# Kernel optimization log

Hardware: AMD Instinct MI355X
Metric: run time of the kernel (lower is better)

The kernel has to match this reference:

```python
import jax, jax.numpy as jnp
import numpy as np

W_SIZE = 16
WIN = 2 * W_SIZE + 1
OUT_F = 256
MODEL = 512  # output_features * 2


def setup_inputs() -> dict:
    key = jax.random.key(0)
    ks = jax.random.split(key, 7)
    B, T = 4, 2048
    s = 0.02
    return {
        "x": jax.random.normal(ks[0], (B, T, MODEL), jnp.float32),
        "encoder_outputs": jax.random.normal(ks[1], (B, T, OUT_F), jnp.float32),
        # Attention: attn Linear (OUT_F + MODEL -> OUT_F), v Linear (OUT_F -> 1, no bias)
        "W_attn": jax.random.normal(ks[2], (OUT_F + MODEL, OUT_F), jnp.float32) * s,
        "b_attn": jnp.zeros((OUT_F,), jnp.float32),
        "v": jax.random.normal(ks[3], (OUT_F,), jnp.float32) * s,
        # final linear: (MODEL + OUT_F -> OUT_F)
        "W_lin": jax.random.normal(ks[4], (MODEL + OUT_F, OUT_F), jnp.float32) * s,
        "b_lin": jnp.zeros((OUT_F,), jnp.float32),
    }


def _windows(enc):
    B, T, F = enc.shape
    padded = jnp.pad(enc, ((0, 0), (W_SIZE, W_SIZE), (0, 0)))
    idx = jnp.arange(T)[:, None] + jnp.arange(WIN)[None, :]
    return padded[:, idx]


def reference(x, encoder_outputs, W_attn, b_attn, v, W_lin, b_lin):
    win = _windows(encoder_outputs)
    B, T, W, F = win.shape
    # additive (Bahdanau) score: concat(hidden, window) -> Linear -> tanh -> v
    Wh, We = W_attn[:MODEL], W_attn[MODEL:]
    energy = jnp.tanh(
        jnp.einsum('btm,mo->bto', x, Wh)[:, :, None, :]
        + jnp.einsum('btwf,fo->btwo', win, We)
        + b_attn
    )
    scores = jnp.einsum('btwo,o->btw', energy, v)
    a = jax.nn.softmax(scores, axis=-1)
    weighted = jnp.einsum('btw,btwf->btf', a, win)        # [B, T, F]
    h = jnp.concatenate([x, weighted], axis=-1)           # [B, T, MODEL+F]
    out = jax.nn.sigmoid(jnp.einsum('btk,ko->bto', h, W_lin) + b_lin)
    return out, a[:, :, None, :]
```

## Files before the change

kernel.cpp:

```cpp
#include <hip/hip_runtime.h>
#include <math.h>

#define T_DIM 2048
#define B_DIM 4
#define BT (B_DIM * T_DIM)
#define MODEL 512
#define OUTF 256
#define WSZ 16
#define WIN 33

#define BM 128
#define BN 128
#define BK 32

#define TB 16
#define HALO 48
#define TS 72

#define ESCALE 2.885390081777927f
#define ECLAMP 30.0f

typedef __attribute__((ext_vector_type(8))) short bf16x8;
typedef __attribute__((ext_vector_type(4))) float f32x4;

__device__ inline unsigned short f2bf(float f) {
  unsigned int u = __float_as_uint(f);
  u += 0x7fffu + ((u >> 16) & 1u);
  return (unsigned short)(u >> 16);
}
__device__ inline float bflo(unsigned int u) {
  return __uint_as_float(u << 16);
}
__device__ inline float bfhi(unsigned int u) {
  return __uint_as_float(u & 0xffff0000u);
}
__device__ inline float bfs(unsigned short u) {
  return __uint_as_float(((unsigned int)u) << 16);
}
__device__ inline float fast_sigmoid(float z) {
  return __builtin_amdgcn_rcpf(1.f + __expf(-z));
}

template <int KS, int MODE>
__device__ __forceinline__ void gemm_body(
    unsigned short (*As)[BM * 40], unsigned short (*Bs)[BN * 40], int rb,
    const float* __restrict__ A, int lda,
    const float* __restrict__ W_attn, const float* __restrict__ W_lin,
    const float* __restrict__ b_attn, const float* __restrict__ b_lin,
    unsigned short* __restrict__ outb, unsigned short* __restrict__ outb2) {
  const int tid = threadIdx.x;
  const int cbg = rb >> 6, rp = rb & 63;
  const int row0 = rp * BM;
  const float* Wsrc = (cbg < 2) ? W_attn : W_lin;
  const int colw = (cbg & 1) * 128;
  constexpr int wrow0 = (MODE == 0) ? 0 : 512;

  const int arow = tid >> 2, akp = (tid & 3) * 8;
  const int brow = tid >> 4, bcp = (tid & 15) * 8;
  const int bkey = (bcp >> 3) & 3;
  const float* aptr = A + (size_t)(row0 + arow) * lda + akp;
  const float* bptr = Wsrc + (size_t)(wrow0 + brow) * OUTF + colw + bcp;

  float4 ra0[2], ra1[2], rb0[2], rb1[2];
  auto LOADS = [&](int sl, int ks) {
    const float* ap = aptr + ks * BK;
    ra0[sl] = *(const float4*)ap;
    ra1[sl] = *(const float4*)(ap + 4);
    const float* bp = bptr + (size_t)ks * BK * OUTF;
    rb0[sl] = *(const float4*)bp;
    rb1[sl] = *(const float4*)(bp + 4);
  };
  auto WRITE = [&](int sl, int buf) {
    unsigned short t[8] = {f2bf(ra0[sl].x), f2bf(ra0[sl].y), f2bf(ra0[sl].z),
                           f2bf(ra0[sl].w), f2bf(ra1[sl].x), f2bf(ra1[sl].y),
                           f2bf(ra1[sl].z), f2bf(ra1[sl].w)};
    *(uint4*)&As[buf][arow * 40 + akp] = *(const uint4*)t;
    const int bk = brow ^ (bkey << 3);
    Bs[buf][(bcp + 0) * 40 + bk] = f2bf(rb0[sl].x);
    Bs[buf][(bcp + 1) * 40 + bk] = f2bf(rb0[sl].y);
    Bs[buf][(bcp + 2) * 40 + bk] = f2bf(rb0[sl].z);
    Bs[buf][(bcp + 3) * 40 + bk] = f2bf(rb0[sl].w);
    Bs[buf][(bcp + 4) * 40 + bk] = f2bf(rb1[sl].x);
    Bs[buf][(bcp + 5) * 40 + bk] = f2bf(rb1[sl].y);
    Bs[buf][(bcp + 6) * 40 + bk] = f2bf(rb1[sl].z);
    Bs[buf][(bcp + 7) * 40 + bk] = f2bf(rb1[sl].w);
  };

  const int w = tid >> 6, lane = tid & 63;
  const int lr = lane & 15, kg = lane >> 4;
  const int rbase = (w & 3) * 32;
  const int cbase = (w >> 2) * 64;
  int bo[4];
#pragma unroll
  for (int f = 0; f < 4; ++f) {
    const int bc = cbase + f * 16 + lr;
    bo[f] = bc * 40 + ((kg ^ ((bc >> 3) & 3)) << 3);
  }

  f32x4 acc[2][4];
#pragma unroll
  for (int m = 0; m < 2; ++m)
#pragma unroll
    for (int f = 0; f < 4; ++f) acc[m][f] = {0.f, 0.f, 0.f, 0.f};

  LOADS(0, 0);
  if (KS > 1) LOADS(1, 1);
  WRITE(0, 0);
  __syncthreads();

#pragma unroll
  for (int ks = 0; ks < KS; ++ks) {
    if (ks + 2 < KS) LOADS(ks & 1, ks + 2);
    const int bf = ks & 1;
    bf16x8 a0 = *(const bf16x8*)&As[bf][(rbase + lr) * 40 + kg * 8];
    bf16x8 a1 = *(const bf16x8*)&As[bf][(rbase + 16 + lr) * 40 + kg * 8];
#pragma unroll
    for (int f = 0; f < 4; ++f) {
      bf16x8 bb = *(const bf16x8*)&Bs[bf][bo[f]];
      acc[0][f] = __builtin_amdgcn_mfma_f32_16x16x32_bf16(a0, bb, acc[0][f], 0, 0, 0);
      acc[1][f] = __builtin_amdgcn_mfma_f32_16x16x32_bf16(a1, bb, acc[1][f], 0, 0, 0);
    }
    if (ks + 1 < KS) WRITE((ks + 1) & 1, (ks + 1) & 1);
    __syncthreads();
  }

#pragma unroll
  for (int m = 0; m < 2; ++m) {
#pragma unroll
    for (int f = 0; f < 4; ++f) {
      const int col = (cbg & 1) * 128 + cbase + f * 16 + lr;
#pragma unroll
      for (int r = 0; r < 4; ++r) {
        const int row = row0 + rbase + m * 16 + kg * 4 + r;
        const float val = acc[m][f][r];
        if (MODE == 0) {
          if (cbg < 2) {
            const float y = fminf((val + b_attn[col]) * ESCALE, ECLAMP);
            outb[(size_t)row * OUTF + col] = f2bf(__builtin_amdgcn_exp2f(y));
          } else {
            outb2[(size_t)row * OUTF + col] = f2bf(val + b_lin[col]);
          }
        } else {
          if (cbg < 2) {
            const float y = fminf(val * ESCALE, ECLAMP);
            outb[(size_t)row * OUTF + col] = f2bf(__builtin_amdgcn_exp2f(y));
          } else {
            outb2[(size_t)row * OUTF + col] = f2bf(val);
          }
        }
      }
    }
  }
}

__global__ __launch_bounds__(512) void gemmAB_kernel(
    const float* __restrict__ x, const float* __restrict__ enc,
    const float* __restrict__ W_attn, const float* __restrict__ W_lin,
    const float* __restrict__ b_attn, const float* __restrict__ b_lin,
    unsigned short* __restrict__ xwe2, unsigned short* __restrict__ z1b,
    unsigned short* __restrict__ ewe2, unsigned short* __restrict__ encWl2) {
  __shared__ unsigned short As[2][BM * 40];
  __shared__ unsigned short Bs[2][BN * 40];
  if (blockIdx.x < 256)
    gemm_body<16, 0>(As, Bs, blockIdx.x, x, MODEL, W_attn, W_lin, b_attn,
                     b_lin, xwe2, z1b);
  else
    gemm_body<8, 1>(As, Bs, blockIdx.x - 256, enc, OUTF, W_attn, W_lin,
                    nullptr, nullptr, ewe2, encWl2);
}

__global__ __launch_bounds__(512) void attn_gemmc_kernel(
    const unsigned short* __restrict__ xwe2,
    const unsigned short* __restrict__ ewe2,
    const unsigned short* __restrict__ encWl2, const float* __restrict__ v,
    const unsigned short* __restrict__ z1b, float* __restrict__ out,
    float* __restrict__ a_out) {
  __shared__ unsigned short EwT[256 * TS];
  __shared__ unsigned short Ab[TB * TS];

  const int tid = threadIdx.x;
  const int wv = tid >> 6, lane = tid & 63;
  const int rb = ((blockIdx.x & 7) << 6) | (blockIdx.x >> 3);
  const int t0 = rb * TB;
  const int b = t0 >> 11;
  const int tloc = t0 & (T_DIM - 1);
  const int g = lane >> 4, sl = lane & 15;

  if (tid < TB * TS / 8) ((uint4*)Ab)[tid] = make_uint4(0, 0, 0, 0);
  {
    const int col = tid >> 1, off = 48 + (tid & 1) * 8;
    const int kswz = ((col >> 3) & 7) << 3;
    *(uint4*)&EwT[col * TS + (off ^ kswz)] = make_uint4(0, 0, 0, 0);
  }

  for (int u = tid; u < HALO * 32; u += 512) {
    const int r = u >> 5, s = u & 31;
    const int tg = tloc - WSZ + r;
    uint4 qw = make_uint4(0, 0, 0, 0);
    if ((unsigned)tg < T_DIM)
      qw = *(const uint4*)(encWl2 + (((size_t)(b * T_DIM + tg)) << 8) + s * 8);
    unsigned short tt[8];
    *(uint4*)tt = qw;
    const int rsw = r ^ ((s & 7) << 3);
#pragma unroll
    for (int j = 0; j < 8; ++j) EwT[(s * 8 + j) * TS + rsw] = tt[j];
  }

  float vf[16];
  {
    const float4* vp = (const float4*)(v + sl * 16);
#pragma unroll
    for (int j = 0; j < 4; ++j) {
      float4 t4 = vp[j];
      vf[4 * j] = t4.x; vf[4 * j + 1] = t4.y;
      vf[4 * j + 2] = t4.z; vf[4 * j + 3] = t4.w;
    }
  }
  __syncthreads();

  const int lrow = wv * 2;
  const int bt0 = t0 + lrow, bt1 = bt0 + 1;

  float xe0[16], xe1[16];
  {
    const uint4* xp0 = (const uint4*)(xwe2 + ((size_t)bt0 << 8) + sl * 16);
    const uint4* xp1 = (const uint4*)(xwe2 + ((size_t)bt1 << 8) + sl * 16);
    uint4 q0 = xp0[0], q1 = xp0[1], q2 = xp1[0], q3 = xp1[1];
    unsigned int u0[8] = {q0.x, q0.y, q0.z, q0.w, q1.x, q1.y, q1.z, q1.w};
    unsigned int u1[8] = {q2.x, q2.y, q2.z, q2.w, q3.x, q3.y, q3.z, q3.w};
#pragma unroll
    for (int j = 0; j < 8; ++j) {
      xe0[2 * j] = bflo(u0[j]); xe0[2 * j + 1] = bfhi(u0[j]);
      xe1[2 * j] = bflo(u1[j]); xe1[2 * j + 1] = bfhi(u1[j]);
    }
  }

  const size_t bbase = ((size_t)(b * T_DIM)) << 8;
  const int tb0 = tloc + lrow - WSZ;
  float s0 = 0.f, s1 = 0.f;
#pragma unroll
  for (int c = 0; c < 9; ++c) {
    const int w_ = c * 4 + g;
    const int tg0 = tb0 + w_, tg1 = tg0 + 1;
    const bool vr0 = ((unsigned)tg0 < T_DIM);
    const bool vr1 = ((unsigned)tg1 < T_DIM);
    const uint4* p0 =
        (const uint4*)(ewe2 + bbase + (((size_t)(vr0 ? tg0 : 0)) << 8) + sl * 16);
    const uint4* p1 =
        (const uint4*)(ewe2 + bbase + (((size_t)(vr1 ? tg1 : 0)) << 8) + sl * 16);
    uint4 a0q = p0[0], a1q = p0[1];
    uint4 b0q = p1[0], b1q = p1[1];
    const uint4 ones =
        make_uint4(0x3f803f80u, 0x3f803f80u, 0x3f803f80u, 0x3f803f80u);
    if (!vr0) { a0q = ones; a1q = ones; }
    if (!vr1) { b0q = ones; b1q = ones; }
    unsigned int e0[8] = {a0q.x, a0q.y, a0q.z, a0q.w, a1q.x, a1q.y, a1q.z, a1q.w};
    unsigned int e1[8] = {b0q.x, b0q.y, b0q.z, b0q.w, b1q.x, b1q.y, b1q.z, b1q.w};
    float acc0 = 0.f, acc1 = 0.f;
#pragma unroll
    for (int j = 0; j < 8; ++j) {
      const float v0 = vf[2 * j], v1 = vf[2 * j + 1];
      const float vsj = v0 + v1;
      {
        const float E0 = xe0[2 * j] * bflo(e0[j]);
        const float E1 = xe0[2 * j + 1] * bfhi(e0[j]);
        const float den = (E0 + 1.f) * (E1 + 1.f);
        float num = fmaf(v0, E1, vsj);
        num = fmaf(v1, E0, num);
        acc0 = fmaf(num, __builtin_amdgcn_rcpf(den), acc0);
      }
      {
        const float E0 = xe1[2 * j] * bflo(e1[j]);
        const float E1 = xe1[2 * j + 1] * bfhi(e1[j]);
        const float den = (E0 + 1.f) * (E1 + 1.f);
        float num = fmaf(v0, E1, vsj);
        num = fmaf(v1, E0, num);
        acc1 = fmaf(num, __builtin_amdgcn_rcpf(den), acc1);
      }
    }
#pragma unroll
    for (int off = 1; off < 16; off <<= 1) {
      acc0 += __shfl_xor(acc0, off);
      acc1 += __shfl_xor(acc1, off);
    }
    const int src = (lane & 3) << 4;
    float c0v = __shfl(acc0, src), c1v = __shfl(acc1, src);
    if ((lane >> 2) == c) { s0 = c0v; s1 = c1v; }
  }

  float p0 = (lane < WIN) ? __builtin_amdgcn_exp2f(-ESCALE * s0) : 0.f;
  float p1 = (lane < WIN) ? __builtin_amdgcn_exp2f(-ESCALE * s1) : 0.f;
  float q0 = p0, q1 = p1;
#pragma unroll
  for (int off = 1; off < 64; off <<= 1) {
    q0 += __shfl_xor(q0, off);
    q1 += __shfl_xor(q1, off);
  }
  const float a0v = p0 * __builtin_amdgcn_rcpf(q0);
  const float a1v = p1 * __builtin_amdgcn_rcpf(q1);
  if (lane < WIN) {
    a_out[(size_t)bt0 * WIN + lane] = a0v;
    a_out[(size_t)bt1 * WIN + lane] = a1v;
    Ab[lrow * TS + lrow + lane] = f2bf(a0v);
    Ab[(lrow + 1) * TS + (lrow + 1) + lane] = f2bf(a1v);
  }
  __syncthreads();

  const int lr = lane & 15, kg = lane >> 4;
  f32x4 acc[2] = {{0.f, 0.f, 0.f, 0.f}, {0.f, 0.f, 0.f, 0.f}};
#pragma unroll
  for (int ks = 0; ks < 2; ++ks) {
    bf16x8 a = *(const bf16x8*)&Ab[lr * TS + ks * 32 + kg * 8];
#pragma unroll
    for (int f = 0; f < 2; ++f) {
      const int colB = wv * 32 + f * 16 + lr;
      const int kswz = ((colB >> 3) & 7) << 3;
      bf16x8 bb = *(const bf16x8*)&EwT[colB * TS + ((ks * 32 + kg * 8) ^ kswz)];
      acc[f] = __builtin_amdgcn_mfma_f32_16x16x32_bf16(a, bb, acc[f], 0, 0, 0);
    }
  }
#pragma unroll
  for (int f = 0; f < 2; ++f) {
    const int col = wv * 32 + f * 16 + lr;
#pragma unroll
    for (int r = 0; r < 4; ++r) {
      const int row = t0 + kg * 4 + r;
      out[(size_t)row * OUTF + col] = fast_sigmoid(
          acc[f][r] + bfs(z1b[(size_t)row * OUTF + col]));
    }
  }
}

extern "C" void kernel_launch(void* const* d_in, const int* in_sizes, int n_in,
                              void* d_out, int out_size, void* d_ws,
                              size_t ws_size, hipStream_t stream) {
  const float* x      = (const float*)d_in[0];
  const float* enc    = (const float*)d_in[1];
  const float* W_attn = (const float*)d_in[2];
  const float* b_attn = (const float*)d_in[3];
  const float* v      = (const float*)d_in[4];
  const float* W_lin  = (const float*)d_in[5];
  const float* b_lin  = (const float*)d_in[6];

  float* out   = (float*)d_out;
  float* a_out = out + (size_t)BT * OUTF;

  unsigned short* xwe2   = (unsigned short*)d_ws;
  unsigned short* ewe2   = xwe2 + (size_t)BT * OUTF;
  unsigned short* encWl2 = ewe2 + (size_t)BT * OUTF;
  unsigned short* z1b    = encWl2 + (size_t)BT * OUTF;

  gemmAB_kernel<<<512, 512, 0, stream>>>(x, enc, W_attn, W_lin, b_attn,
                                         b_lin, xwe2, z1b, ewe2, encWl2);
  attn_gemmc_kernel<<<512, 512, 0, stream>>>(xwe2, ewe2, encWl2, v, z1b,
                                             out, a_out);
}
```

Measured before the change: 43.73 us.

## Remap attention score computation to one lane per window position

Reworks the score stage so each lane owns one window position (32 positions for two rows per wave) and loops over all 256 features serially, instead of 16-lane groups splitting the feature dimension and reducing with shuffles over 9 chunks. The x-projection row and v/paired-v vectors are staged in shared memory, and the 33rd window position is handled by a separate 16-lane reduction. This removes most cross-lane shuffle reductions and the wasted lanes of the 9x4 chunking, but each lane now makes strided global row reads and the kernel uses more LDS.

```diff
diff --git a/kernel.cpp b/kernel.cpp
--- a/kernel.cpp
+++ b/kernel.cpp
@@ -177,6 +177,9 @@
     float* __restrict__ a_out) {
   __shared__ unsigned short EwT[256 * TS];
   __shared__ unsigned short Ab[TB * TS];
+  __shared__ unsigned short Xe[TB * 256];
+  __shared__ float Vs[256];
+  __shared__ float Vp[128];
 
   const int tid = threadIdx.x;
   const int wv = tid >> 6, lane = tid & 63;
@@ -184,7 +187,6 @@
   const int t0 = rb * TB;
   const int b = t0 >> 11;
   const int tloc = t0 & (T_DIM - 1);
-  const int g = lane >> 4, sl = lane & 15;
 
   if (tid < TB * TS / 8) ((uint4*)Ab)[tid] = make_uint4(0, 0, 0, 0);
   {
@@ -205,104 +207,144 @@
 #pragma unroll
     for (int j = 0; j < 8; ++j) EwT[(s * 8 + j) * TS + rsw] = tt[j];
   }
-
-  float vf[16];
   {
-    const float4* vp = (const float4*)(v + sl * 16);
-#pragma unroll
-    for (int j = 0; j < 4; ++j) {
-      float4 t4 = vp[j];
-      vf[4 * j] = t4.x; vf[4 * j + 1] = t4.y;
-      vf[4 * j + 2] = t4.z; vf[4 * j + 3] = t4.w;
-    }
-  }
+    const int row = tid >> 5, seg = tid & 31;
+    *(uint4*)&Xe[row * 256 + seg * 8] =
+        *(const uint4*)(xwe2 + (((size_t)(t0 + row)) << 8) + seg * 8);
+  }
+  if (tid < 256) Vs[tid] = v[tid];
+  if (tid < 128) Vp[tid] = v[2 * tid] + v[2 * tid + 1];
   __syncthreads();
 
-  const int lrow = wv * 2;
-  const int bt0 = t0 + lrow, bt1 = bt0 + 1;
-
-  float xe0[16], xe1[16];
+  const size_t bbase = ((size_t)(b * T_DIM)) << 8;
+  const uint4 ones =
+      make_uint4(0x3f803f80u, 0x3f803f80u, 0x3f803f80u, 0x3f803f80u);
+
+  const int p = lane >> 5;
+  const int wA = (lane & 31) + 1;
+  const int lrow = wv * 2 + p;
+  const int bt = t0 + lrow;
+
+  float S = 0.f;
   {
-    const uint4* xp0 = (const uint4*)(xwe2 + ((size_t)bt0 << 8) + sl * 16);
-    const uint4* xp1 = (const uint4*)(xwe2 + ((size_t)bt1 << 8) + sl * 16);
-    uint4 q0 = xp0[0], q1 = xp0[1], q2 = xp1[0], q3 = xp1[1];
-    unsigned int u0[8] = {q0.x, q0.y, q0.z, q0.w, q1.x, q1.y, q1.z, q1.w};
-    unsigned int u1[8] = {q2.x, q2.y, q2.z, q2.w, q3.x, q3.y, q3.z, q3.w};
-#pragma unroll
-    for (int j = 0; j < 8; ++j) {
-      xe0[2 * j] = bflo(u0[j]); xe0[2 * j + 1] = bfhi(u0[j]);
-      xe1[2 * j] = bflo(u1[j]); xe1[2 * j + 1] = bfhi(u1[j]);
-    }
-  }
-
-  const size_t bbase = ((size_t)(b * T_DIM)) << 8;
-  const int tb0 = tloc + lrow - WSZ;
-  float s0 = 0.f, s1 = 0.f;
-#pragma unroll
-  for (int c = 0; c < 9; ++c) {
-    const int w_ = c * 4 + g;
-    const int tg0 = tb0 + w_, tg1 = tg0 + 1;
-    const bool vr0 = ((unsigned)tg0 < T_DIM);
-    const bool vr1 = ((unsigned)tg1 < T_DIM);
-    const uint4* p0 =
-        (const uint4*)(ewe2 + bbase + (((size_t)(vr0 ? tg0 : 0)) << 8) + sl * 16);
-    const uint4* p1 =
-        (const uint4*)(ewe2 + bbase + (((size_t)(vr1 ? tg1 : 0)) << 8) + sl * 16);
-    uint4 a0q = p0[0], a1q = p0[1];
-    uint4 b0q = p1[0], b1q = p1[1];
-    const uint4 ones =
-        make_uint4(0x3f803f80u, 0x3f803f80u, 0x3f803f80u, 0x3f803f80u);
-    if (!vr0) { a0q = ones; a1q = ones; }
-    if (!vr1) { b0q = ones; b1q = ones; }
-    unsigned int e0[8] = {a0q.x, a0q.y, a0q.z, a0q.w, a1q.x, a1q.y, a1q.z, a1q.w};
-    unsigned int e1[8] = {b0q.x, b0q.y, b0q.z, b0q.w, b1q.x, b1q.y, b1q.z, b1q.w};
-    float acc0 = 0.f, acc1 = 0.f;
-#pragma unroll
-    for (int j = 0; j < 8; ++j) {
-      const float v0 = vf[2 * j], v1 = vf[2 * j + 1];
-      const float vsj = v0 + v1;
-      {
-        const float E0 = xe0[2 * j] * bflo(e0[j]);
-        const float E1 = xe0[2 * j + 1] * bfhi(e0[j]);
-        const float den = (E0 + 1.f) * (E1 + 1.f);
-        float num = fmaf(v0, E1, vsj);
-        num = fmaf(v1, E0, num);
-        acc0 = fmaf(num, __builtin_amdgcn_rcpf(den), acc0);
-      }
-      {
-        const float E0 = xe1[2 * j] * bflo(e1[j]);
-        const float E1 = xe1[2 * j + 1] * bfhi(e1[j]);
-        const float den = (E0 + 1.f) * (E1 + 1.f);
-        float num = fmaf(v0, E1, vsj);
-        num = fmaf(v1, E0, num);
-        acc1 = fmaf(num, __builtin_amdgcn_rcpf(den), acc1);
-      }
-    }
-#pragma unroll
-    for (int off = 1; off < 16; off <<= 1) {
-      acc0 += __shfl_xor(acc0, off);
-      acc1 += __shfl_xor(acc1, off);
-    }
-    const int src = (lane & 3) << 4;
-    float c0v = __shfl(acc0, src), c1v = __shfl(acc1, src);
-    if ((lane >> 2) == c) { s0 = c0v; s1 = c1v; }
-  }
-
-  float p0 = (lane < WIN) ? __builtin_amdgcn_exp2f(-ESCALE * s0) : 0.f;
-  float p1 = (lane < WIN) ? __builtin_amdgcn_exp2f(-ESCALE * s1) : 0.f;
-  float q0 = p0, q1 = p1;
-#pragma unroll
-  for (int off = 1; off < 64; off <<= 1) {
-    q0 += __shfl_xor(q0, off);
-    q1 += __shfl_xor(q1, off);
-  }
-  const float a0v = p0 * __builtin_amdgcn_rcpf(q0);
-  const float a1v = p1 * __builtin_amdgcn_rcpf(q1);
-  if (lane < WIN) {
-    a_out[(size_t)bt0 * WIN + lane] = a0v;
-    a_out[(size_t)bt1 * WIN + lane] = a1v;
-    Ab[lrow * TS + lrow + lane] = f2bf(a0v);
-    Ab[(lrow + 1) * TS + (lrow + 1) + lane] = f2bf(a1v);
+    const int trow = tloc + lrow + wA - WSZ;
+    const bool vld = ((unsigned)trow < T_DIM);
+    const unsigned short* ewp =
+        ewe2 + bbase + (((size_t)(vld ? trow : 0)) << 8);
+#pragma unroll 4
+    for (int g = 0; g < 32; ++g) {
+      uint4 q = *(const uint4*)(ewp + g * 8);
+      if (!vld) q = ones;
+      const uint4 xq = *(const uint4*)&Xe[lrow * 256 + g * 8];
+      const float4 va = *(const float4*)&Vs[g * 8];
+      const float4 vb = *(const float4*)&Vs[g * 8 + 4];
+      const float4 vp4 = *(const float4*)&Vp[g * 4];
+      {
+        const float E0 = bflo(xq.x) * bflo(q.x);
+        const float E1 = bfhi(xq.x) * bfhi(q.x);
+        const float den = (E0 + 1.f) * (E1 + 1.f);
+        float num = fmaf(va.x, E1, vp4.x);
+        num = fmaf(va.y, E0, num);
+        S = fmaf(num, __builtin_amdgcn_rcpf(den), S);
+      }
+      {
+        const float E0 = bflo(xq.y) * bflo(q.y);
+        const float E1 = bfhi(xq.y) * bfhi(q.y);
+        const float den = (E0 + 1.f) * (E1 + 1.f);
+        float num = fmaf(va.z, E1, vp4.y);
+        num = fmaf(va.w, E0, num);
+        S = fmaf(num, __builtin_amdgcn_rcpf(den), S);
+      }
+      {
+        const float E0 = bflo(xq.z) * bflo(q.z);
+        const float E1 = bfhi(xq.z) * bfhi(q.z);
+        const float den = (E0 + 1.f) * (E1 + 1.f);
+        float num = fmaf(vb.x, E1, vp4.z);
+        num = fmaf(vb.y, E0, num);
+        S = fmaf(num, __builtin_amdgcn_rcpf(den), S);
+      }
+      {
+        const float E0 = bflo(xq.w) * bflo(q.w);
+        const float E1 = bfhi(xq.w) * bfhi(q.w);
+        const float den = (E0 + 1.f) * (E1 + 1.f);
+        float num = fmaf(vb.z, E1, vp4.w);
+        num = fmaf(vb.w, E0, num);
+        S = fmaf(num, __builtin_amdgcn_rcpf(den), S);
+      }
+    }
+  }
+
+  float accm = 0.f;
+  {
+    const int grp = lane >> 4, slm = lane & 15;
+    const int lrm = wv * 2 + (grp & 1);
+    const int t2 = tloc + lrm - WSZ;
+    const bool vl2 = ((unsigned)t2 < T_DIM);
+    const unsigned short* ep =
+        ewe2 + bbase + (((size_t)(vl2 ? t2 : 0)) << 8) + slm * 16;
+    uint4 qa = *(const uint4*)ep;
+    uint4 qb = *(const uint4*)(ep + 8);
+    if (!vl2) { qa = ones; qb = ones; }
+#pragma unroll
+    for (int jg = 0; jg < 2; ++jg) {
+      const int gi = slm * 2 + jg;
+      const uint4 qq = jg ? qb : qa;
+      const uint4 xq = *(const uint4*)&Xe[lrm * 256 + gi * 8];
+      const float4 va = *(const float4*)&Vs[gi * 8];
+      const float4 vb = *(const float4*)&Vs[gi * 8 + 4];
+      const float4 vp4 = *(const float4*)&Vp[gi * 4];
+      {
+        const float E0 = bflo(xq.x) * bflo(qq.x);
+        const float E1 = bfhi(xq.x) * bfhi(qq.x);
+        const float den = (E0 + 1.f) * (E1 + 1.f);
+        float num = fmaf(va.x, E1, vp4.x);
+        num = fmaf(va.y, E0, num);
+        accm = fmaf(num, __builtin_amdgcn_rcpf(den), accm);
+      }
+      {
+        const float E0 = bflo(xq.y) * bflo(qq.y);
+        const float E1 = bfhi(xq.y) * bfhi(qq.y);
+        const float den = (E0 + 1.f) * (E1 + 1.f);
+        float num = fmaf(va.z, E1, vp4.y);
+        num = fmaf(va.w, E0, num);
+        accm = fmaf(num, __builtin_amdgcn_rcpf(den), accm);
+      }
+      {
+        const float E0 = bflo(xq.z) * bflo(qq.z);
+        const float E1 = bfhi(xq.z) * bfhi(qq.z);
+        const float den = (E0 + 1.f) * (E1 + 1.f);
+        float num = fmaf(vb.x, E1, vp4.z);
+        num = fmaf(vb.y, E0, num);
+        accm = fmaf(num, __builtin_amdgcn_rcpf(den), accm);
+      }
+      {
+        const float E0 = bflo(xq.w) * bflo(qq.w);
+        const float E1 = bfhi(xq.w) * bfhi(qq.w);
+        const float den = (E0 + 1.f) * (E1 + 1.f);
+        float num = fmaf(vb.z, E1, vp4.w);
+        num = fmaf(vb.w, E0, num);
+        accm = fmaf(num, __builtin_amdgcn_rcpf(den), accm);
+      }
+    }
+#pragma unroll
+    for (int off = 1; off < 16; off <<= 1) accm += __shfl_xor(accm, off);
+  }
+
+  const float S0 = __shfl(accm, p << 4);
+  const float pw = __builtin_amdgcn_exp2f(-ESCALE * S);
+  const float pz = __builtin_amdgcn_exp2f(-ESCALE * S0);
+  float sum = pw;
+#pragma unroll
+  for (int off = 1; off < 32; off <<= 1) sum += __shfl_xor(sum, off);
+  sum += pz;
+  const float rs = __builtin_amdgcn_rcpf(sum);
+  const float aw = pw * rs;
+  a_out[(size_t)bt * WIN + wA] = aw;
+  Ab[lrow * TS + lrow + wA] = f2bf(aw);
+  if ((lane & 31) == 0) {
+    const float a0 = pz * rs;
+    a_out[(size_t)bt * WIN] = a0;
+    Ab[lrow * TS + lrow] = f2bf(a0);
   }
   __syncthreads();
 
@@ -325,8 +367,8 @@
 #pragma unroll
     for (int r = 0; r < 4; ++r) {
       const int row = t0 + kg * 4 + r;
-      out[(size_t)row * OUTF + col] = fast_sigmoid(
-          acc[f][r] + bfs(z1b[(size_t)row * OUTF + col]));
+      out[(size_t)row * OUTF + col] =
+          fast_sigmoid(acc[f][r] + bfs(z1b[(size_t)row * OUTF + col]));
     }
   }
 }
```

Measured after the change: 46.25 us. +5.8%, slower.
